# Optimization experiments

Measured on AMD Instinct MI355X. Metric: run time of the kernel, lower is better.

Reference implementation:

```python
import jax, jax.numpy as jnp
import numpy as np
from jax import lax

THRESHOLD = 0.9


def _conv(x, w, b, stride):
    # x: [B,C,H,W], w: [O,I,3,3] (OIHW)
    y = lax.conv_general_dilated(x, w, (stride, stride), 'SAME',
                                 dimension_numbers=('NCHW', 'OIHW', 'NCHW'))
    return y + b[None, :, None, None]


def _expert(x, w1, b1, w2, b2, wf, bf):
    h = jax.nn.relu(_conv(x, w1, b1, 2))   # [B,64,112,112]
    h = jax.nn.relu(_conv(h, w2, b2, 2))   # [B,128,56,56]
    g = h.mean(axis=(2, 3))                # [B,128] global average pool
    return g @ wf + bf                     # [B,2] logits


def setup_inputs() -> dict:
    key = jax.random.key(0)
    ks = jax.random.split(key, 13)
    f32 = jnp.float32
    def rn(k, shape, scale):
        return jax.random.normal(k, shape, dtype=f32) * scale
    return {
        'x':    rn(ks[0], (64, 3, 224, 224), 1.0),
        't_w1': rn(ks[1], (64, 3, 3, 3),   0.2),
        't_b1': jnp.zeros((64,), f32),
        't_w2': rn(ks[2], (128, 64, 3, 3), 0.05),
        't_b2': jnp.zeros((128,), f32),
        't_wf': rn(ks[3], (128, 2),        0.1),
        't_bf': jnp.zeros((2,), f32),
        'f_w1': rn(ks[4], (64, 3, 3, 3),   0.2),
        'f_b1': jnp.zeros((64,), f32),
        'f_w2': rn(ks[5], (128, 64, 3, 3), 0.05),
        'f_b2': jnp.zeros((128,), f32),
        'f_wf': rn(ks[6], (128, 2),        0.1),
        'f_bf': jnp.zeros((2,), f32),
    }


def reference(x, t_w1, t_b1, t_w2, t_b2, t_wf, t_bf,
              f_w1, f_b1, f_w2, f_b2, f_wf, f_bf):
    t_logits = _expert(x, t_w1, t_b1, t_w2, t_b2, t_wf, t_bf)   # [B,2]
    t_conf = jax.nn.softmax(t_logits, axis=1).max(axis=1)        # [B]
    use_texture2 = t_conf <= THRESHOLD                           # [B] bool
    # jit-friendly dense evaluation of the second expert; the where-mask
    # reproduces the original gather/scatter blend exactly (values and grads).
    f_logits = _expert(x, f_w1, f_b1, f_w2, f_b2, f_wf, f_bf)   # [B,2]
    output = jnp.where(use_texture2[:, None],
                       0.7 * t_logits + 0.3 * f_logits,
                       t_logits)
    freq_usage = use_texture2.astype(jnp.float32).mean()
    return (output, freq_usage)
```

## Files before the change

kernel.cpp:

```cpp
#include <hip/hip_runtime.h>
#include <hip/hip_fp16.h>
#include <math.h>


#define W2B_OFF   0ull
#define W1F_OFF   294912ull
#define G_OFF     303104ull
#define H1_OFF    368640ull
#define H1E_US    52301824ull
#define H1B_US    817216ull
#define WS_NEED   (H1_OFF + 2ull*H1E_US*2ull + 4096ull)

typedef __attribute__((ext_vector_type(8))) short bf16x8;
typedef __attribute__((ext_vector_type(8))) _Float16 half8;
typedef __attribute__((ext_vector_type(4))) float f32x4;

__device__ inline ushort f2h(float v) {
  __half h = __float2half(v);
  return *(ushort*)&h;
}

__global__ __launch_bounds__(256) void prep_new(
    const float* __restrict__ w2_t, const float* __restrict__ w2_f,
    const float* __restrict__ w1_t, const float* __restrict__ w1_f,
    char* __restrict__ ws) {
  int idx = blockIdx.x * 256 + threadIdx.x;
  ushort* w2frag = (ushort*)(ws + W2B_OFF);
  ushort* w1frag = (ushort*)(ws + W1F_OFF);
  if (idx < 147456) {
    int j    = idx & 7;
    int lane = (idx >> 3) & 63;
    int t2   = idx >> 9;
    int kc   = t2 % 18;
    int t3   = t2 / 18;
    int octile = t3 & 7;
    int e    = t3 >> 3;
    int oc = octile * 16 + (lane & 15);
    int kk = kc * 32 + (lane >> 4) * 8 + j;
    int kh = kk / 192, r2 = kk - kh * 192, kw = r2 >> 6, ic = r2 & 63;
    const float* src = e ? w2_f : w2_t;
    w2frag[idx] = f2h(src[((oc * 64 + ic) * 3 + kh) * 3 + kw]);
  } else if (idx < 147456 + 4096) {
    int i2   = idx - 147456;
    int j    = i2 & 7;
    int lane = (i2 >> 3) & 63;
    int m    = (i2 >> 9) & 3;
    int e    = (i2 >> 11) & 1;
    int oc = m * 16 + (lane & 15);
    int kk = (lane >> 4) * 8 + j;
    const float* src = e ? w1_f : w1_t;
    w1frag[i2] = f2h((kk < 27) ? src[oc * 27 + kk] : 0.f);
  }
}

__global__ __launch_bounds__(256) void conv1_mfma(
    const float* __restrict__ x,
    const ushort* __restrict__ w1f_all,
    const float* __restrict__ b1_t, const float* __restrict__ b1_f,
    ushort* __restrict__ h1_all)
{
  const int gR  = blockIdx.x;
  const int b   = blockIdx.y;
  const int e   = blockIdx.z;
  const int tid = threadIdx.x;
  const int w    = tid >> 6;
  const int lane = tid & 63;
  const int q    = lane >> 4;
  const int n    = lane & 15;

  ushort* h1b = h1_all + (size_t)e * H1E_US + (size_t)b * H1B_US;
  const float* b1 = e ? b1_f : b1_t;

  constexpr int CW = 233;
  __shared__ unsigned int xs[3 * 9 * CW];

  const float* xb = x + (size_t)b * 150528;
  const int xr0 = 8 * gR;
  for (int i = tid; i < 1512; i += 256) {
    int ic  = i / 504;
    int rem = i - ic * 504;
    int r   = rem / 56;
    int u   = rem - r * 56;
    int xr  = xr0 + r;
    float4 p = make_float4(0.f, 0.f, 0.f, 0.f);
    if (xr < 224) p = *(const float4*)(xb + (ic * 224 + xr) * 224 + 4 * u);
    int base = (ic * 9 + r) * CW + 4 * u;
    xs[base + 0] = (unsigned int)f2h(p.x);
    xs[base + 1] = (unsigned int)f2h(p.y);
    xs[base + 2] = (unsigned int)f2h(p.z);
    xs[base + 3] = (unsigned int)f2h(p.w);
  }
  if (tid < 27) xs[tid * CW + 224] = 0;

  h1b[((size_t)((4 * gR + (tid >> 6)) * 113 + 112)) * 64 + (tid & 63)] = 0;
  if (gR == 0) {
    unsigned int* z = (unsigned int*)&h1b[(size_t)112 * 113 * 64];
    for (int i = tid; i < 3616; i += 256) z[i] = 0;
  }

  half8 wf[4];
#pragma unroll
  for (int m = 0; m < 4; ++m)
    wf[m] = *(const half8*)&w1f_all[(((size_t)(e * 4 + m)) * 64 + lane) * 8];
  float4 bv[4];
#pragma unroll
  for (int m = 0; m < 4; ++m)
    bv[m] = *(const float4*)&b1[m * 16 + 4 * q];

  int off[8];
#pragma unroll
  for (int j = 0; j < 8; ++j) {
    int kk = q * 8 + j;
    if (kk < 27) {
      int ic = kk / 9;
      int r9 = kk - ic * 9;
      int kh = r9 / 3;
      int kw = r9 - kh * 3;
      off[j] = (ic * 9 + kh) * CW + kw;
    } else {
      off[j] = -1;
    }
  }

  __syncthreads();

  const int row   = 4 * gR + w;
  const int rbase = (2 * w) * CW;

  for (int nt = 0; nt < 7; ++nt) {
    const int c = nt * 16 + n;
    const int base = rbase + 2 * c;
    unsigned int g[8];
#pragma unroll
    for (int j = 0; j < 8; ++j)
      g[j] = (off[j] >= 0) ? xs[base + off[j]] : 0u;
    union { half8 h; unsigned int u[4]; } bh;
#pragma unroll
    for (int p = 0; p < 4; ++p)
      bh.u[p] = (g[2 * p] & 0xffffu) | (g[2 * p + 1] << 16);
    f32x4 acc[4];
#pragma unroll
    for (int m = 0; m < 4; ++m) acc[m] = (f32x4){0.f, 0.f, 0.f, 0.f};
#pragma unroll
    for (int m = 0; m < 4; ++m)
      acc[m] = __builtin_amdgcn_mfma_f32_16x16x32_f16(wf[m], bh.h, acc[m], 0, 0, 0);
    size_t po = ((size_t)(row * 113 + c)) * 64 + 4 * q;
#pragma unroll
    for (int m = 0; m < 4; ++m) {
      ushort v0 = f2h(fmaxf(acc[m][0] + bv[m].x, 0.f));
      ushort v1 = f2h(fmaxf(acc[m][1] + bv[m].y, 0.f));
      ushort v2 = f2h(fmaxf(acc[m][2] + bv[m].z, 0.f));
      ushort v3 = f2h(fmaxf(acc[m][3] + bv[m].w, 0.f));
      uint2 uu;
      uu.x = (unsigned int)v0 | ((unsigned int)v1 << 16);
      uu.y = (unsigned int)v2 | ((unsigned int)v3 << 16);
      *(uint2*)&h1b[po + m * 16] = uu;
    }
  }
}

__global__ __launch_bounds__(256) void conv2_mfma(
    const ushort* __restrict__ h1_all,
    const ushort* __restrict__ w2frag,
    const float* __restrict__ b2_t, const float* __restrict__ b2_f,
    float* __restrict__ g)
{
  const int T = blockIdx.x;
  const int b = blockIdx.y;
  const int e = blockIdx.z;
  const int tid  = threadIdx.x;
  const int w    = tid >> 6;
  const int lane = tid & 63;
  const ushort* h1b = h1_all + (size_t)e * H1E_US + (size_t)b * H1B_US;
  const float* b2 = e ? b2_f : b2_t;

  __shared__ ushort hs[2 * 113 * 72];

  const int q   = lane >> 4;
  const int n   = lane & 15;
  const int pxl = lane & 7;
  const int rl  = (lane >> 3) & 1;

  f32x4 acc[2][7];
#pragma unroll
  for (int mt = 0; mt < 2; ++mt)
#pragma unroll
    for (int nt = 0; nt < 7; ++nt) acc[mt][nt] = (f32x4){0.f, 0.f, 0.f, 0.f};

  for (int kh = 0; kh < 3; ++kh) {
    __syncthreads();
    for (int i = tid; i < 1808; i += 256) {
      int rs = (i >= 904) ? 1 : 0;
      int rem = i - rs * 904;
      int hx = rem >> 3, gq = rem & 7;
      int R = 4 * T + kh + 2 * rs;
      int gsw = gq ^ ((hx >> 1) & 7);
      *(bf16x8*)&hs[(rs * 113 + hx) * 72 + 8 * gsw] =
          *(const bf16x8*)&h1b[((size_t)(R * 113 + hx)) * 64 + 8 * gq];
    }
    __syncthreads();
#pragma unroll
    for (int kw = 0; kw < 3; ++kw) {
#pragma unroll
      for (int icc = 0; icc < 2; ++icc) {
        const int kc = kh * 6 + kw * 2 + icc;
        half8 bf[7];
#pragma unroll
        for (int nt = 0; nt < 7; ++nt) {
          int hx = 2 * (8 * nt + pxl) + kw;
          int gr = (icc * 4 + q) ^ ((hx >> 1) & 7);
          bf[nt] = *(const half8*)&hs[(rl * 113 + hx) * 72 + 8 * gr];
        }
#pragma unroll
        for (int mt = 0; mt < 2; ++mt) {
          const int octile = 2 * w + mt;
          half8 af = *(const half8*)
              &w2frag[((size_t)((e * 8 + octile) * 18 + kc)) * 512 + lane * 8];
#pragma unroll
          for (int nt = 0; nt < 7; ++nt)
            acc[mt][nt] = __builtin_amdgcn_mfma_f32_16x16x32_f16(
                af, bf[nt], acc[mt][nt], 0, 0, 0);
        }
      }
    }
  }

#pragma unroll
  for (int mt = 0; mt < 2; ++mt) {
#pragma unroll
    for (int reg = 0; reg < 4; ++reg) {
      const int oc = 32 * w + 16 * mt + 4 * q + reg;
      const float bias = b2[oc];
      float s = 0.f;
#pragma unroll
      for (int nt = 0; nt < 7; ++nt) s += fmaxf(acc[mt][nt][reg] + bias, 0.f);
      s += __shfl_xor(s, 1);
      s += __shfl_xor(s, 2);
      s += __shfl_xor(s, 4);
      s += __shfl_xor(s, 8);
      if (n == 0) atomicAdd(&g[((size_t)e * 64 + b) * 128 + oc], s);
    }
  }
}

__global__ __launch_bounds__(64) void finale(
    const float* __restrict__ g,
    const float* __restrict__ t_wf, const float* __restrict__ t_bf,
    const float* __restrict__ f_wf, const float* __restrict__ f_bf,
    float* __restrict__ out)
{
  const int b = threadIdx.x;
  const float inv = 1.0f / 3136.0f;
  const float* gt = g + b * 128;
  const float* gf = g + (64 + b) * 128;
  float lt0 = t_bf[0], lt1 = t_bf[1];
  float lf0 = f_bf[0], lf1 = f_bf[1];
  for (int k = 0; k < 128; ++k) {
    float vt = gt[k] * inv;
    float vf = gf[k] * inv;
    lt0 = fmaf(vt, t_wf[2 * k],     lt0);
    lt1 = fmaf(vt, t_wf[2 * k + 1], lt1);
    lf0 = fmaf(vf, f_wf[2 * k],     lf0);
    lf1 = fmaf(vf, f_wf[2 * k + 1], lf1);
  }
  float m  = fmaxf(lt0, lt1);
  float e0 = expf(lt0 - m), e1 = expf(lt1 - m);
  float conf = fmaxf(e0, e1) / (e0 + e1);
  bool use2 = (conf <= 0.9f);
  out[2 * b]     = use2 ? 0.7f * lt0 + 0.3f * lf0 : lt0;
  out[2 * b + 1] = use2 ? 0.7f * lt1 + 0.3f * lf1 : lt1;
  unsigned long long mask = __ballot(use2);
  if (b == 0) out[128] = (float)__popcll(mask) * (1.0f / 64.0f);
}

__global__ __launch_bounds__(256) void transpose_w2(
    const float* __restrict__ w2_t, const float* __restrict__ w2_f,
    float* __restrict__ w2t) {
  int idx = blockIdx.x * 256 + threadIdx.x;
  int e = idx / 73728;
  int r = idx - e * 73728;
  int k = r >> 7, oc = r & 127;
  const float* src = e ? w2_f : w2_t;
  w2t[idx] = src[oc * 576 + k];
}

__global__ __launch_bounds__(256, 3) void fused_expert(
    const float* __restrict__ x,
    const float* __restrict__ w1_t, const float* __restrict__ b1_t,
    const float* __restrict__ b2_t,
    const float* __restrict__ w1_f, const float* __restrict__ b1_f,
    const float* __restrict__ b2_f,
    const float* __restrict__ w2t_all, float* __restrict__ g)
{
  const int tile = blockIdx.x, b = blockIdx.y, e = blockIdx.z;
  const int ty = tile >> 1, tx = tile & 1;
  const float* w1  = e ? w1_f : w1_t;
  const float* b1  = e ? b1_f : b1_t;
  const float* b2  = e ? b2_f : b2_t;
  const float* w2t = w2t_all + e * 73728;
  __shared__ float x_s[3 * 19 * 116];
  __shared__ float h1_s[8 * 9 * 58];
  __shared__ float w1_s[1728];
  const int tid = threadIdx.x;
  {
    const float* xb = x + (size_t)b * 150528;
    const int xr0 = ty * 16, xc0 = tx * 112;
    for (int idx = tid; idx < 3 * 19 * 116; idx += 256) {
      int ic = idx / (19 * 116);
      int rem = idx - ic * (19 * 116);
      int r = rem / 116, cc = rem - r * 116;
      int xr = xr0 + r, xc = xc0 + cc;
      float v = 0.f;
      if (xr < 224 && xc < 224 && cc < 115) v = xb[(ic * 224 + xr) * 224 + xc];
      x_s[idx] = v;
    }
    for (int idx = tid; idx < 1728; idx += 256) w1_s[idx] = w1[idx];
  }
  const int ocg = tid >> 4, posg = tid & 15;
  int pbase[7];
#pragma unroll
  for (int j = 0; j < 7; ++j) {
    int p = posg + 16 * j, py = p / 28, px = p - py * 28;
    pbase[j] = py * 2 * 58 + px * 2;
  }
  float acc[7][8];
#pragma unroll
  for (int j = 0; j < 7; ++j)
#pragma unroll
    for (int i = 0; i < 8; ++i) acc[j][i] = 0.f;
  const int hc_l = tid >> 5, l32 = tid & 31;
  for (int c = 0; c < 8; ++c) {
    __syncthreads();
    {
      const int hc = c * 8 + hc_l;
      const float bias = b1[hc];
      float wr[27];
#pragma unroll
      for (int qq = 0; qq < 27; ++qq) wr[qq] = w1_s[hc * 27 + qq];
      for (int p = l32; p < 513; p += 32) {
        int hy = p / 57, hx = p - hy * 57;
        float a = bias;
#pragma unroll
        for (int ic = 0; ic < 3; ++ic)
#pragma unroll
          for (int kh = 0; kh < 3; ++kh) {
            const float* row = &x_s[ic * (19 * 116) + (2 * hy + kh) * 116 + 2 * hx];
            a = fmaf(row[0], wr[ic * 9 + kh * 3 + 0], a);
            a = fmaf(row[1], wr[ic * 9 + kh * 3 + 1], a);
            a = fmaf(row[2], wr[ic * 9 + kh * 3 + 2], a);
          }
        float v = fmaxf(a, 0.f);
        int hy_g = ty * 8 + hy, hx_g = tx * 56 + hx;
        if (hy_g >= 112 || hx_g >= 112) v = 0.f;
        h1_s[hc_l * 522 + hy * 58 + hx] = v;
      }
    }
    __syncthreads();
    for (int ic_l = 0; ic_l < 8; ++ic_l) {
#pragma unroll
      for (int kh = 0; kh < 3; ++kh)
#pragma unroll
        for (int kw = 0; kw < 3; ++kw) {
          const int k = (c * 8 + ic_l) * 9 + kh * 3 + kw;
          const float4 wA = *(const float4*)(w2t + k * 128 + ocg * 8);
          const float4 wB = *(const float4*)(w2t + k * 128 + ocg * 8 + 4);
          const float* hp = &h1_s[ic_l * 522 + kh * 58 + kw];
#pragma unroll
          for (int j = 0; j < 7; ++j) {
            float h = hp[pbase[j]];
            acc[j][0] = fmaf(wA.x, h, acc[j][0]);
            acc[j][1] = fmaf(wA.y, h, acc[j][1]);
            acc[j][2] = fmaf(wA.z, h, acc[j][2]);
            acc[j][3] = fmaf(wA.w, h, acc[j][3]);
            acc[j][4] = fmaf(wB.x, h, acc[j][4]);
            acc[j][5] = fmaf(wB.y, h, acc[j][5]);
            acc[j][6] = fmaf(wB.z, h, acc[j][6]);
            acc[j][7] = fmaf(wB.w, h, acc[j][7]);
          }
        }
    }
  }
  __syncthreads();
  float* red = x_s;
#pragma unroll
  for (int i = 0; i < 8; ++i) {
    float bb = b2[ocg * 8 + i];
    float t = 0.f;
#pragma unroll
    for (int j = 0; j < 7; ++j) t += fmaxf(acc[j][i] + bb, 0.f);
    red[posg * 129 + ocg * 8 + i] = t;
  }
  __syncthreads();
  if (tid < 128) {
    float t = 0.f;
#pragma unroll
    for (int pg = 0; pg < 16; ++pg) t += red[pg * 129 + tid];
    atomicAdd(&g[(e * 64 + b) * 128 + tid], t);
  }
}

extern "C" void kernel_launch(void* const* d_in, const int* in_sizes, int n_in,
                              void* d_out, int out_size, void* d_ws, size_t ws_size,
                              hipStream_t stream) {
  const float* x    = (const float*)d_in[0];
  const float* t_w1 = (const float*)d_in[1];
  const float* t_b1 = (const float*)d_in[2];
  const float* t_w2 = (const float*)d_in[3];
  const float* t_b2 = (const float*)d_in[4];
  const float* t_wf = (const float*)d_in[5];
  const float* t_bf = (const float*)d_in[6];
  const float* f_w1 = (const float*)d_in[7];
  const float* f_b1 = (const float*)d_in[8];
  const float* f_w2 = (const float*)d_in[9];
  const float* f_b2 = (const float*)d_in[10];
  const float* f_wf = (const float*)d_in[11];
  const float* f_bf = (const float*)d_in[12];
  float* out = (float*)d_out;
  char* ws = (char*)d_ws;

  if (ws_size >= WS_NEED) {
    float*  gbuf   = (float*)(ws + G_OFF);
    ushort* h1     = (ushort*)(ws + H1_OFF);
    ushort* w2frag = (ushort*)(ws + W2B_OFF);
    ushort* w1f    = (ushort*)(ws + W1F_OFF);
    hipMemsetAsync(gbuf, 0, 2 * 64 * 128 * sizeof(float), stream);
    prep_new<<<592, 256, 0, stream>>>(t_w2, f_w2, t_w1, f_w1, ws);
    conv1_mfma<<<dim3(28, 64, 2), 256, 0, stream>>>(x, w1f, t_b1, f_b1, h1);
    conv2_mfma<<<dim3(28, 64, 2), 256, 0, stream>>>(h1, w2frag, t_b2, f_b2, gbuf);
    finale<<<1, 64, 0, stream>>>(gbuf, t_wf, t_bf, f_wf, f_bf, out);
  } else {
    float* w2t = (float*)ws;
    float* g2  = (float*)(ws + 589824);
    hipMemsetAsync(g2, 0, 2 * 64 * 128 * sizeof(float), stream);
    transpose_w2<<<576, 256, 0, stream>>>(t_w2, f_w2, w2t);
    fused_expert<<<dim3(28, 64, 2), 256, 0, stream>>>(
        x, t_w1, t_b1, t_b2, f_w1, f_b1, f_b2, w2t, g2);
    finale<<<1, 64, 0, stream>>>(g2, t_wf, t_bf, f_wf, f_bf, out);
  }
}
```

Measured before the change: 296.9 us.

## Enlarge conv2 tile to four output rows with 2x2 warp layout

Each conv2 block now covers four output rows instead of two, and its four waves are arranged as a 2x2 grid over output channels and rows. Each wave handles 64 channels, so weight fragments loaded from global memory are reused across twice as many pixels, and the grid shrinks from 28 to 14 row tiles. The XOR swizzle on the shared-memory layout is removed, which may bring back LDS bank conflicts. Doubling the accumulators to 4x7 MFMA tiles raises register pressure and lowers occupancy.

```diff
diff --git a/kernel.cpp b/kernel.cpp
--- a/kernel.cpp
+++ b/kernel.cpp
@@ -170,32 +170,34 @@
   const int e = blockIdx.z;
   const int tid  = threadIdx.x;
   const int w    = tid >> 6;
+  const int wm   = w & 1;
+  const int wn   = w >> 1;
   const int lane = tid & 63;
   const ushort* h1b = h1_all + (size_t)e * H1E_US + (size_t)b * H1B_US;
   const float* b2 = e ? b2_f : b2_t;
 
-  __shared__ ushort hs[2 * 113 * 72];
-
-  const int q   = lane >> 4;
+  __shared__ ushort hs[4 * 113 * 72];
+
+  const int q   = (lane >> 4) & 3;
   const int n   = lane & 15;
   const int pxl = lane & 7;
   const int rl  = (lane >> 3) & 1;
-
-  f32x4 acc[2][7];
-#pragma unroll
-  for (int mt = 0; mt < 2; ++mt)
-#pragma unroll
-    for (int nt = 0; nt < 7; ++nt) acc[mt][nt] = (f32x4){0.f, 0.f, 0.f, 0.f};
+  const int s   = 2 * wn + rl;
+
+  f32x4 acc[4][7];
+#pragma unroll
+  for (int m = 0; m < 4; ++m)
+#pragma unroll
+    for (int nt = 0; nt < 7; ++nt) acc[m][nt] = (f32x4){0.f, 0.f, 0.f, 0.f};
 
   for (int kh = 0; kh < 3; ++kh) {
     __syncthreads();
-    for (int i = tid; i < 1808; i += 256) {
-      int rs = (i >= 904) ? 1 : 0;
-      int rem = i - rs * 904;
+    for (int i = tid; i < 3616; i += 256) {
+      int ss  = i / 904;
+      int rem = i - ss * 904;
       int hx = rem >> 3, gq = rem & 7;
-      int R = 4 * T + kh + 2 * rs;
-      int gsw = gq ^ ((hx >> 1) & 7);
-      *(bf16x8*)&hs[(rs * 113 + hx) * 72 + 8 * gsw] =
+      int R = 8 * T + kh + 2 * ss;
+      *(bf16x8*)&hs[(ss * 113 + hx) * 72 + 8 * gq] =
           *(const bf16x8*)&h1b[((size_t)(R * 113 + hx)) * 64 + 8 * gq];
     }
     __syncthreads();
@@ -208,37 +210,36 @@
 #pragma unroll
         for (int nt = 0; nt < 7; ++nt) {
           int hx = 2 * (8 * nt + pxl) + kw;
-          int gr = (icc * 4 + q) ^ ((hx >> 1) & 7);
-          bf[nt] = *(const half8*)&hs[(rl * 113 + hx) * 72 + 8 * gr];
+          bf[nt] = *(const half8*)&hs[(s * 113 + hx) * 72 + icc * 32 + 8 * q];
         }
 #pragma unroll
-        for (int mt = 0; mt < 2; ++mt) {
-          const int octile = 2 * w + mt;
+        for (int m = 0; m < 4; ++m) {
+          const int octile = 4 * wm + m;
           half8 af = *(const half8*)
               &w2frag[((size_t)((e * 8 + octile) * 18 + kc)) * 512 + lane * 8];
 #pragma unroll
           for (int nt = 0; nt < 7; ++nt)
-            acc[mt][nt] = __builtin_amdgcn_mfma_f32_16x16x32_f16(
-                af, bf[nt], acc[mt][nt], 0, 0, 0);
+            acc[m][nt] = __builtin_amdgcn_mfma_f32_16x16x32_f16(
+                af, bf[nt], acc[m][nt], 0, 0, 0);
         }
       }
     }
   }
 
 #pragma unroll
-  for (int mt = 0; mt < 2; ++mt) {
+  for (int m = 0; m < 4; ++m) {
 #pragma unroll
     for (int reg = 0; reg < 4; ++reg) {
-      const int oc = 32 * w + 16 * mt + 4 * q + reg;
+      const int oc = 64 * wm + 16 * m + 4 * q + reg;
       const float bias = b2[oc];
-      float s = 0.f;
-#pragma unroll
-      for (int nt = 0; nt < 7; ++nt) s += fmaxf(acc[mt][nt][reg] + bias, 0.f);
-      s += __shfl_xor(s, 1);
-      s += __shfl_xor(s, 2);
-      s += __shfl_xor(s, 4);
-      s += __shfl_xor(s, 8);
-      if (n == 0) atomicAdd(&g[((size_t)e * 64 + b) * 128 + oc], s);
+      float sacc = 0.f;
+#pragma unroll
+      for (int nt = 0; nt < 7; ++nt) sacc += fmaxf(acc[m][nt][reg] + bias, 0.f);
+      sacc += __shfl_xor(sacc, 1);
+      sacc += __shfl_xor(sacc, 2);
+      sacc += __shfl_xor(sacc, 4);
+      sacc += __shfl_xor(sacc, 8);
+      if (n == 0) atomicAdd(&g[((size_t)e * 64 + b) * 128 + oc], sacc);
     }
   }
 }
@@ -426,7 +427,7 @@
     hipMemsetAsync(gbuf, 0, 2 * 64 * 128 * sizeof(float), stream);
     prep_new<<<592, 256, 0, stream>>>(t_w2, f_w2, t_w1, f_w1, ws);
     conv1_mfma<<<dim3(28, 64, 2), 256, 0, stream>>>(x, w1f, t_b1, f_b1, h1);
-    conv2_mfma<<<dim3(28, 64, 2), 256, 0, stream>>>(h1, w2frag, t_b2, f_b2, gbuf);
+    conv2_mfma<<<dim3(14, 64, 2), 256, 0, stream>>>(h1, w2frag, t_b2, f_b2, gbuf);
     finale<<<1, 64, 0, stream>>>(gbuf, t_wf, t_bf, f_wf, f_bf, out);
   } else {
     float* w2t = (float*)ws;
```

After: 376.6 us. 1.27x slower.

## Stage all five conv2 input rows in LDS once and vectorize conv1 stores

Applied to the files above, without the earlier changes.

conv2 now loads all five input rows for its tile into shared memory in a single batched pass, with a new XOR swizzle and no padding. This replaces the per-kh reload of two rows between barriers and removes repeated global traffic and synchronisation. conv1 writes each lane's 16 channels as two contiguous 16-byte stores, and the conv2 weight fragments use a matching input-channel permutation. LDS use grows to about 72KB per block, which may lower occupancy.

```diff
diff --git a/kernel.cpp b/kernel.cpp
--- a/kernel.cpp
+++ b/kernel.cpp
@@ -37,9 +37,10 @@
     int e    = t3 >> 3;
     int oc = octile * 16 + (lane & 15);
     int kk = kc * 32 + (lane >> 4) * 8 + j;
-    int kh = kk / 192, r2 = kk - kh * 192, kw = r2 >> 6, ic = r2 & 63;
+    int kh = kk / 192, r2 = kk - kh * 192, kw = r2 >> 6, slot = r2 & 63;
+    int icp = ((slot >> 2) & 3) * 16 + ((slot >> 4) & 3) * 4 + (slot & 3);
     const float* src = e ? w2_f : w2_t;
-    w2frag[idx] = f2h(src[((oc * 64 + ic) * 3 + kh) * 3 + kw]);
+    w2frag[idx] = f2h(src[((oc * 64 + icp) * 3 + kh) * 3 + kw]);
   } else if (idx < 147456 + 4096) {
     int i2   = idx - 147456;
     int j    = i2 & 7;
@@ -144,18 +145,17 @@
 #pragma unroll
     for (int m = 0; m < 4; ++m)
       acc[m] = __builtin_amdgcn_mfma_f32_16x16x32_f16(wf[m], bh.h, acc[m], 0, 0, 0);
-    size_t po = ((size_t)(row * 113 + c)) * 64 + 4 * q;
+    size_t po = ((size_t)(row * 113 + c)) * 64 + q * 16;
+    union { ushort us[16]; uint4 v4[2]; } pk;
 #pragma unroll
     for (int m = 0; m < 4; ++m) {
-      ushort v0 = f2h(fmaxf(acc[m][0] + bv[m].x, 0.f));
-      ushort v1 = f2h(fmaxf(acc[m][1] + bv[m].y, 0.f));
-      ushort v2 = f2h(fmaxf(acc[m][2] + bv[m].z, 0.f));
-      ushort v3 = f2h(fmaxf(acc[m][3] + bv[m].w, 0.f));
-      uint2 uu;
-      uu.x = (unsigned int)v0 | ((unsigned int)v1 << 16);
-      uu.y = (unsigned int)v2 | ((unsigned int)v3 << 16);
-      *(uint2*)&h1b[po + m * 16] = uu;
-    }
+      pk.us[m * 4 + 0] = f2h(fmaxf(acc[m][0] + bv[m].x, 0.f));
+      pk.us[m * 4 + 1] = f2h(fmaxf(acc[m][1] + bv[m].y, 0.f));
+      pk.us[m * 4 + 2] = f2h(fmaxf(acc[m][2] + bv[m].z, 0.f));
+      pk.us[m * 4 + 3] = f2h(fmaxf(acc[m][3] + bv[m].w, 0.f));
+    }
+    *(uint4*)&h1b[po]     = pk.v4[0];
+    *(uint4*)&h1b[po + 8] = pk.v4[1];
   }
 }
 
@@ -174,13 +174,35 @@
   const ushort* h1b = h1_all + (size_t)e * H1E_US + (size_t)b * H1B_US;
   const float* b2 = e ? b2_f : b2_t;
 
-  __shared__ ushort hs[2 * 113 * 72];
+  __shared__ ushort hs[5 * 113 * 64];
 
   const int q   = lane >> 4;
   const int n   = lane & 15;
   const int pxl = lane & 7;
   const int rl  = (lane >> 3) & 1;
 
+#pragma unroll
+  for (int half = 0; half < 2; ++half) {
+    bf16x8 tmp[9];
+    int dst[9];
+    bool ok[9];
+#pragma unroll
+    for (int k = 0; k < 9; ++k) {
+      int s = tid + (half * 9 + k) * 256;
+      ok[k] = (s < 4520);
+      int r = s / 904;
+      int rem = s - 904 * r;
+      int hx = rem >> 3, gq = rem & 7;
+      if (ok[k])
+        tmp[k] = *(const bf16x8*)&h1b[((size_t)((4 * T + r) * 113 + hx)) * 64 + 8 * gq];
+      dst[k] = (r * 113 + hx) * 64 + 8 * (gq ^ (hx & 7));
+    }
+#pragma unroll
+    for (int k = 0; k < 9; ++k)
+      if (ok[k]) *(bf16x8*)&hs[dst[k]] = tmp[k];
+  }
+  __syncthreads();
+
   f32x4 acc[2][7];
 #pragma unroll
   for (int mt = 0; mt < 2; ++mt)
@@ -188,28 +210,18 @@
     for (int nt = 0; nt < 7; ++nt) acc[mt][nt] = (f32x4){0.f, 0.f, 0.f, 0.f};
 
   for (int kh = 0; kh < 3; ++kh) {
-    __syncthreads();
-    for (int i = tid; i < 1808; i += 256) {
-      int rs = (i >= 904) ? 1 : 0;
-      int rem = i - rs * 904;
-      int hx = rem >> 3, gq = rem & 7;
-      int R = 4 * T + kh + 2 * rs;
-      int gsw = gq ^ ((hx >> 1) & 7);
-      *(bf16x8*)&hs[(rs * 113 + hx) * 72 + 8 * gsw] =
-          *(const bf16x8*)&h1b[((size_t)(R * 113 + hx)) * 64 + 8 * gq];
-    }
-    __syncthreads();
+    const int rbase = (kh + 2 * rl) * 113 * 64;
 #pragma unroll
     for (int kw = 0; kw < 3; ++kw) {
 #pragma unroll
       for (int icc = 0; icc < 2; ++icc) {
         const int kc = kh * 6 + kw * 2 + icc;
+        const int gsw = 8 * ((icc * 4 + q) ^ ((2 * pxl + kw) & 7));
         half8 bf[7];
 #pragma unroll
         for (int nt = 0; nt < 7; ++nt) {
           int hx = 2 * (8 * nt + pxl) + kw;
-          int gr = (icc * 4 + q) ^ ((hx >> 1) & 7);
-          bf[nt] = *(const half8*)&hs[(rl * 113 + hx) * 72 + 8 * gr];
+          bf[nt] = *(const half8*)&hs[rbase + hx * 64 + gsw];
         }
 #pragma unroll
         for (int mt = 0; mt < 2; ++mt) {
```

After: 245.4 us. 17.4% less time.
